# Kernel optimization log

Measured on AMD Instinct MI355X. Metric: run time of the kernel, lower is better.

## Reference

```python
import jax, jax.numpy as jnp
import numpy as np

B, S, E, H = 8, 2048, 256, 8
LN_EPS = 1e-5


def setup_inputs() -> dict:
    key = jax.random.key(0)
    ks = jax.random.split(key, 5)
    x = jax.random.normal(ks[0], (B, S, E), dtype=jnp.float32)
    Wq = jax.random.normal(ks[1], (E, E), dtype=jnp.float32) * 0.02
    Wk = jax.random.normal(ks[2], (E, E), dtype=jnp.float32) * 0.02
    Wv = jax.random.normal(ks[3], (E, E), dtype=jnp.float32) * 0.02
    bias_table = jax.random.normal(ks[4], (2 * S - 1, H), dtype=jnp.float32) * 0.02
    ln_gamma = jnp.ones((E,), dtype=jnp.float32)
    ln_beta = jnp.zeros((E,), dtype=jnp.float32)
    return {"x": x, "Wq": Wq, "Wk": Wk, "Wv": Wv,
            "bias_table": bias_table, "ln_gamma": ln_gamma, "ln_beta": ln_beta}


def reference(x, Wq, Wk, Wv, bias_table, ln_gamma, ln_beta):
    b, s, e = x.shape
    h = bias_table.shape[1]
    d = e // h
    scale = e ** (-0.5)  # note: original scales by emb_size**-0.5, not head_dim

    # torch nn.Linear(bias=False): y = x @ W.T
    q = (x @ Wq.T).reshape(b, s, h, d).transpose(0, 2, 1, 3)  # [b,h,s,d]
    k = (x @ Wk.T).reshape(b, s, h, d).transpose(0, 2, 1, 3)
    v = (x @ Wv.T).reshape(b, s, h, d).transpose(0, 2, 1, 3)

    # full attention matrix (the chunked torch loop computes exactly this)
    attn = jax.nn.softmax(jnp.einsum('bhqd,bhkd->bhqk', q, k) * scale, axis=-1)

    # relative bias: index[i,j] = i - j + (s-1); added AFTER softmax (faithful)
    idx = jnp.arange(s)[:, None] - jnp.arange(s)[None, :] + (s - 1)  # [s,s]
    rel_bias = bias_table[idx].transpose(2, 0, 1)  # [h,s,s]
    attn = attn + rel_bias[None]

    out = jnp.einsum('bhqk,bhkd->bhqd', attn, v)
    out = out.transpose(0, 2, 1, 3).reshape(b, s, e)

    # LayerNorm over last dim
    mu = jnp.mean(out, axis=-1, keepdims=True)
    var = jnp.var(out, axis=-1, keepdims=True)
    out = (out - mu) * jax.lax.rsqrt(var + LN_EPS) * ln_gamma + ln_beta
    return out
```

## Files before the change

### kernel.cpp

```cpp
#include <hip/hip_runtime.h>
#include <math.h>

typedef unsigned short u16;
typedef unsigned int u32;
typedef __attribute__((ext_vector_type(8))) short short8;
typedef __attribute__((ext_vector_type(16))) float floatx16;

constexpr int CB = 8;
constexpr int CS = 2048;
constexpr int CE = 256;
constexpr int CH = 8;
constexpr int CD = 32;
constexpr float CLN_EPS = 1e-5f;
constexpr float QSC = 0.0625f * 1.44269504088896341f;

constexpr int QP = 40;
constexpr int VP2 = 136;
constexpr int XP = 264;
constexpr int RST = 4104;

__device__ inline u32 fbits(float f) { union { float f; u32 u; } c; c.f = f; return c.u; }
__device__ inline u32 pack2(float a, float b) {
  return __builtin_amdgcn_perm(fbits(b) + 0x8000u, fbits(a) + 0x8000u, 0x07060302u);
}
__device__ inline u16 bf1(float a) { return (u16)((fbits(a) + 0x8000u) >> 16); }
__device__ inline short8 ld8(const u16* p) {
  union { uint4 q; short8 v; } c; c.q = *(const uint4*)p; return c.v;
}

#if __has_builtin(__builtin_amdgcn_permlane32_swap)
__device__ inline void swap32(u32& a, u32& b) {
  typedef __attribute__((ext_vector_type(2))) unsigned int uint2v;
  uint2v r = __builtin_amdgcn_permlane32_swap(a, b, false, false);
  a = r[0]; b = r[1];
}
#else
__device__ inline void swap32(u32& a, u32& b) {
  int hi = (threadIdx.x >> 5) & 1;
  u32 sa = (u32)__shfl_xor((int)a, 32);
  u32 sb = (u32)__shfl_xor((int)b, 32);
  u32 na = hi ? sb : a;
  u32 nb = hi ? b : sa;
  a = na; b = nb;
}
#endif

__global__ __launch_bounds__(256) void prep_kernel(
    const float* __restrict__ Wq, const float* __restrict__ Wk,
    const float* __restrict__ Wv, const float* __restrict__ table,
    u16* __restrict__ Wb, u16* __restrict__ revg) {
  int gid = blockIdx.x * 256 + threadIdx.x;
  if (gid < 49152) {
    int which = gid >> 14;
    int off = (gid & 16383) * 4;
    const float* W = (which == 0) ? Wq : (which == 1) ? Wk : Wv;
    float4 f = *(const float4*)&W[off];
    uint2 o; o.x = pack2(f.x, f.y); o.y = pack2(f.z, f.w);
    *(uint2*)&Wb[(size_t)which * CE * CE + off] = o;
  } else {
    int gid2 = gid - 49152;
    if (gid2 >= 64 * 513) return;
    int g = gid2 / 513;
    int j0 = (gid2 - g * 513) * 8;
    int h = g >> 3, p = g & 7;
    u16 vals[8];
#pragma unroll
    for (int t = 0; t < 8; ++t) {
      int src = 4094 - (j0 + t + p);
      vals[t] = (src >= 0) ? bf1(table[(size_t)src * CH + h]) : (u16)0;
    }
    *(uint4*)&revg[(size_t)g * RST + j0] = *(uint4*)vals;
  }
}

__global__ __launch_bounds__(256, 3) void qkv_mfma_kernel(
    const float* __restrict__ x, const u16* __restrict__ Wb,
    u16* __restrict__ qb, u16* __restrict__ kb, u16* __restrict__ vb) {
  __shared__ __attribute__((aligned(16))) u16 Xs[32 * XP];
  const int m0 = blockIdx.x * 32;
  const int nh = blockIdx.y;
  const int tid = threadIdx.x;
  const int lane = tid & 63, wv = tid >> 6;
  const int lm = lane & 31, lg = lane >> 5;

#pragma unroll
  for (int it = 0; it < 8; ++it) {
    int c = tid + 256 * it;
    int row = c >> 6, f4 = c & 63;
    float4 f = *(const float4*)&x[(size_t)(m0 + row) * CE + f4 * 4];
    uint2 o; o.x = pack2(f.x, f.y); o.y = pack2(f.z, f.w);
    *(uint2*)&Xs[row * XP + f4 * 4] = o;
  }
  __syncthreads();

  const int sg = m0 + lm;
  const int bI = sg >> 11, sI = sg & (CS - 1);

  for (int j = 0; j < 3; ++j) {
    int t = nh * 12 + wv * 3 + j;
    int which = t >> 3;
    int nc = (t & 7) * 32;
    int h = nc >> 5;
    const u16* Wsrc = Wb + (size_t)which * CE * CE;
    floatx16 acc;
#pragma unroll
    for (int i = 0; i < 16; ++i) acc[i] = 0.f;
#pragma unroll
    for (int half = 0; half < 2; ++half) {
      short8 wf[8], xf[8];
#pragma unroll
      for (int kt = 0; kt < 8; ++kt) {
        wf[kt] = ld8(&Wsrc[(size_t)(nc + lm) * CE + (half * 8 + kt) * 16 + lg * 8]);
        xf[kt] = ld8(&Xs[lm * XP + (half * 8 + kt) * 16 + lg * 8]);
      }
#pragma unroll
      for (int kt = 0; kt < 8; ++kt)
        acc = __builtin_amdgcn_mfma_f32_32x32x16_bf16(wf[kt], xf[kt], acc, 0, 0, 0);
    }
    if (which < 2) {
      u16* dst = which ? kb : qb;
      float scl = which ? 1.0f : QSC;
      u32 D[8];
#pragma unroll
      for (int g = 0; g < 8; ++g)
        D[g] = pack2(acc[2 * g] * scl, acc[2 * g + 1] * scl);
      swap32(D[0], D[2]); swap32(D[1], D[3]);
      swap32(D[4], D[6]); swap32(D[5], D[7]);
      size_t base = (((size_t)bI * CH + h) * CS + sI) * CD;
      uint4 U0; U0.x = D[0]; U0.y = D[1]; U0.z = D[2]; U0.w = D[3];
      uint4 U1; U1.x = D[4]; U1.y = D[5]; U1.z = D[6]; U1.w = D[7];
      *(uint4*)&dst[base + 8 * lg] = U0;
      *(uint4*)&dst[base + 16 + 8 * lg] = U1;
    } else {
#pragma unroll
      for (int r = 0; r < 16; ++r) {
        int d = (r & 3) + 8 * (r >> 2) + 4 * lg;
        vb[(((size_t)bI * CH + h) * CD + d) * CS + sI] = bf1(acc[r]);
      }
    }
  }
}

__global__ __launch_bounds__(256, 4) void attn_mfma_kernel(
    const u16* __restrict__ qm, const u16* __restrict__ km,
    const u16* __restrict__ vm, const u16* __restrict__ revg,
    float* __restrict__ out) {
  __shared__ __attribute__((aligned(16))) u16 Ks[2][128 * QP];
  __shared__ __attribute__((aligned(16))) u16 Vt[2][32 * VP2];

  const int q0 = blockIdx.x * 128;
  const int bh = blockIdx.y;
  const int b = bh >> 3, h = bh & 7;
  const int tid = threadIdx.x;
  const int lane = tid & 63, wv = tid >> 6;
  const int lm = lane & 31, lg = lane >> 5;
  const u16* qbp = qm + (size_t)bh * CS * CD;
  const u16* kbp = km + (size_t)bh * CS * CD;
  const u16* vbp = vm + (size_t)bh * CD * CS;

  const int qrow = wv * 32 + lm;
  const u16* qp = qbp + (size_t)(q0 + qrow) * CD;
  short8 qa0 = ld8(qp + lg * 8);
  short8 qa1 = ld8(qp + 16 + lg * 8);

  const int Xb = 2047 - q0 - qrow + lg * 8;
  const int pp = Xb & 7;
  const u16* bp = revg + (size_t)(h * 8 + pp) * RST + (Xb - pp);

  short8 ones;
#pragma unroll
  for (int i = 0; i < 8; ++i) ones[i] = (short)0x3F80;

  const int krow = tid >> 1, kc = (tid & 1) * 16;
  const int vrow = tid >> 3, vc = (tid & 7) * 16;
  uint4 kr0 = *(const uint4*)&kbp[(size_t)krow * CD + kc];
  uint4 kr1 = *(const uint4*)&kbp[(size_t)krow * CD + kc + 8];
  uint4 vr0 = *(const uint4*)&vbp[(size_t)vrow * CS + vc];
  uint4 vr1 = *(const uint4*)&vbp[(size_t)vrow * CS + vc + 8];

  floatx16 acc_e, acc_b, acc_l;
#pragma unroll
  for (int i = 0; i < 16; ++i) { acc_e[i] = 0.f; acc_b[i] = 0.f; acc_l[i] = 0.f; }

  for (int k0 = 0; k0 < CS; k0 += 128) {
    const int p = (k0 >> 7) & 1;
    *(uint4*)&Ks[p][krow * QP + kc] = kr0;
    *(uint4*)&Ks[p][krow * QP + kc + 8] = kr1;
    *(uint4*)&Vt[p][vrow * VP2 + vc] = vr0;
    *(uint4*)&Vt[p][vrow * VP2 + vc + 8] = vr1;
    if (k0 + 128 < CS) {
      kr0 = *(const uint4*)&kbp[(size_t)(k0 + 128 + krow) * CD + kc];
      kr1 = *(const uint4*)&kbp[(size_t)(k0 + 128 + krow) * CD + kc + 8];
      vr0 = *(const uint4*)&vbp[(size_t)vrow * CS + (k0 + 128) + vc];
      vr1 = *(const uint4*)&vbp[(size_t)vrow * CS + (k0 + 128) + vc + 8];
    }
    __syncthreads();

#pragma unroll
    for (int ct = 0; ct < 4; ++ct) {
      uint4 bua = *(const uint4*)&bp[k0 + ct * 32];
      uint4 bub = *(const uint4*)&bp[k0 + ct * 32 + 16];
      short8 a00 = ld8(&Ks[p][(ct * 32 + lm) * QP + lg * 8]);
      short8 a01 = ld8(&Ks[p][(ct * 32 + lm) * QP + 16 + lg * 8]);
      floatx16 sc;
#pragma unroll
      for (int i = 0; i < 16; ++i) sc[i] = 0.f;
      sc = __builtin_amdgcn_mfma_f32_32x32x16_bf16(a00, qa0, sc, 0, 0, 0);
      sc = __builtin_amdgcn_mfma_f32_32x32x16_bf16(a01, qa1, sc, 0, 0, 0);
      u32 P[8];
#pragma unroll
      for (int g = 0; g < 8; ++g) {
        float e0 = __builtin_amdgcn_exp2f(sc[2 * g]);
        float e1 = __builtin_amdgcn_exp2f(sc[2 * g + 1]);
        P[g] = pack2(e0, e1);
      }
      swap32(P[0], P[2]); swap32(P[1], P[3]);
      swap32(P[4], P[6]); swap32(P[5], P[7]);
      union { u32 u[4]; short8 v; } B0, B1;
      B0.u[0] = P[0]; B0.u[1] = P[1]; B0.u[2] = P[2]; B0.u[3] = P[3];
      B1.u[0] = P[4]; B1.u[1] = P[5]; B1.u[2] = P[6]; B1.u[3] = P[7];
      short8 va0 = ld8(&Vt[p][lm * VP2 + ct * 32 + lg * 8]);
      short8 va1 = ld8(&Vt[p][lm * VP2 + ct * 32 + 16 + lg * 8]);
      acc_e = __builtin_amdgcn_mfma_f32_32x32x16_bf16(va0, B0.v, acc_e, 0, 0, 0);
      acc_e = __builtin_amdgcn_mfma_f32_32x32x16_bf16(va1, B1.v, acc_e, 0, 0, 0);
      acc_l = __builtin_amdgcn_mfma_f32_32x32x16_bf16(ones, B0.v, acc_l, 0, 0, 0);
      acc_l = __builtin_amdgcn_mfma_f32_32x32x16_bf16(ones, B1.v, acc_l, 0, 0, 0);
      union { uint4 q; short8 v; } Bb0, Bb1;
      Bb0.q = bua; Bb1.q = bub;
      acc_b = __builtin_amdgcn_mfma_f32_32x32x16_bf16(va0, Bb0.v, acc_b, 0, 0, 0);
      acc_b = __builtin_amdgcn_mfma_f32_32x32x16_bf16(va1, Bb1.v, acc_b, 0, 0, 0);
    }
  }

  float rl = __builtin_amdgcn_rcpf(acc_l[0]);
  size_t ob = ((size_t)b * CS + q0 + qrow) * CE + h * CD;
#pragma unroll
  for (int g = 0; g < 4; ++g) {
    float4 r4;
    r4.x = acc_e[4 * g + 0] * rl + acc_b[4 * g + 0];
    r4.y = acc_e[4 * g + 1] * rl + acc_b[4 * g + 1];
    r4.z = acc_e[4 * g + 2] * rl + acc_b[4 * g + 2];
    r4.w = acc_e[4 * g + 3] * rl + acc_b[4 * g + 3];
    *(float4*)&out[ob + 8 * g + 4 * lg] = r4;
  }
}

__global__ __launch_bounds__(256) void ln_kernel(float* __restrict__ io,
                                                 const float* __restrict__ gamma,
                                                 const float* __restrict__ beta) {
  int tid = threadIdx.x;
  size_t row = (size_t)blockIdx.x * 4 + (tid >> 6);
  int c = (tid & 63) * 4;
  float4 v = *(const float4*)&io[row * CE + c];
  float s1 = v.x + v.y + v.z + v.w;
  float s2 = v.x * v.x + v.y * v.y + v.z * v.z + v.w * v.w;
#pragma unroll
  for (int off = 1; off < 64; off <<= 1) {
    s1 += __shfl_xor(s1, off);
    s2 += __shfl_xor(s2, off);
  }
  float mu = s1 * (1.0f / CE);
  float var = s2 * (1.0f / CE) - mu * mu;
  float rs = rsqrtf(var + CLN_EPS);
  float4 g = *(const float4*)&gamma[c];
  float4 be = *(const float4*)&beta[c];
  float4 o;
  o.x = (v.x - mu) * rs * g.x + be.x;
  o.y = (v.y - mu) * rs * g.y + be.y;
  o.z = (v.z - mu) * rs * g.z + be.z;
  o.w = (v.w - mu) * rs * g.w + be.w;
  *(float4*)&io[row * CE + c] = o;
}

extern "C" void kernel_launch(void* const* d_in, const int* in_sizes, int n_in,
                              void* d_out, int out_size, void* d_ws, size_t ws_size,
                              hipStream_t stream) {
  (void)in_sizes; (void)n_in; (void)out_size; (void)ws_size;
  const float* x          = (const float*)d_in[0];
  const float* Wq         = (const float*)d_in[1];
  const float* Wk         = (const float*)d_in[2];
  const float* Wv         = (const float*)d_in[3];
  const float* bias_table = (const float*)d_in[4];
  const float* gamma      = (const float*)d_in[5];
  const float* beta       = (const float*)d_in[6];
  float* out = (float*)d_out;

  u16* ws = (u16*)d_ws;
  u16* Wb = ws;
  u16* qb = Wb + 3 * CE * CE;
  u16* kb = qb + (size_t)CB * CH * CS * CD;
  u16* vb = kb + (size_t)CB * CH * CS * CD;
  u16* revg = vb + (size_t)CB * CH * CS * CD;

  prep_kernel<<<dim3(321), dim3(256), 0, stream>>>(Wq, Wk, Wv, bias_table, Wb, revg);
  qkv_mfma_kernel<<<dim3(512, 2), dim3(256), 0, stream>>>(x, Wb, qb, kb, vb);
  attn_mfma_kernel<<<dim3(CS / 128, CB * CH), dim3(256), 0, stream>>>(qb, kb, vb, revg, out);
  ln_kernel<<<dim3(CB * CS / 4), dim3(256), 0, stream>>>(out, gamma, beta);
}
```

Baseline: 190.8 us.

## Retile QKV GEMM with staged weights, shrink attention blocks, sum softmax denominator in registers

```diff
diff --git a/kernel.cpp b/kernel.cpp
--- a/kernel.cpp
+++ b/kernel.cpp
@@ -15,8 +15,8 @@
 constexpr float QSC = 0.0625f * 1.44269504088896341f;
 
 constexpr int QP = 40;
-constexpr int VP2 = 136;
-constexpr int XP = 264;
+constexpr int VP = 72;
+constexpr int WP = 264;
 constexpr int RST = 4104;
 
 __device__ inline u32 fbits(float f) { union { float f; u32 u; } c; c.f = f; return c.u; }
@@ -73,50 +73,72 @@
   }
 }
 
-__global__ __launch_bounds__(256, 3) void qkv_mfma_kernel(
+__global__ __launch_bounds__(256, 4) void qkv_mfma_kernel(
     const float* __restrict__ x, const u16* __restrict__ Wb,
     u16* __restrict__ qb, u16* __restrict__ kb, u16* __restrict__ vb) {
-  __shared__ __attribute__((aligned(16))) u16 Xs[32 * XP];
-  const int m0 = blockIdx.x * 32;
-  const int nh = blockIdx.y;
+  __shared__ __attribute__((aligned(16))) u16 Ws[64 * WP];
+  __shared__ __attribute__((aligned(16))) u16 Xs[2][128 * QP];
+  const int m0 = blockIdx.x * 128;
+  const int F0 = blockIdx.y * 64;
   const int tid = threadIdx.x;
   const int lane = tid & 63, wv = tid >> 6;
   const int lm = lane & 31, lg = lane >> 5;
 
-#pragma unroll
-  for (int it = 0; it < 8; ++it) {
-    int c = tid + 256 * it;
-    int row = c >> 6, f4 = c & 63;
-    float4 f = *(const float4*)&x[(size_t)(m0 + row) * CE + f4 * 4];
-    uint2 o; o.x = pack2(f.x, f.y); o.y = pack2(f.z, f.w);
-    *(uint2*)&Xs[row * XP + f4 * 4] = o;
-  }
-  __syncthreads();
-
-  const int sg = m0 + lm;
+  {
+    const u16* Wsrc = Wb + (size_t)(F0 >> 8) * CE * CE + (size_t)(F0 & 255) * CE;
+#pragma unroll
+    for (int c = 0; c < 8; ++c) {
+      int i = tid * 8 + c;
+      int row = i >> 5, col = (i & 31) * 8;
+      *(uint4*)&Ws[row * WP + col] = *(const uint4*)&Wsrc[(size_t)row * CE + col];
+    }
+  }
+
+  const int xrow = tid >> 1, xh = (tid & 1) * 16;
+  const float* xsrc = &x[(size_t)(m0 + xrow) * CE + xh];
+  float4 px0 = *(const float4*)(xsrc + 0);
+  float4 px1 = *(const float4*)(xsrc + 4);
+  float4 px2 = *(const float4*)(xsrc + 8);
+  float4 px3 = *(const float4*)(xsrc + 12);
+
+  floatx16 acc0, acc1;
+#pragma unroll
+  for (int i = 0; i < 16; ++i) { acc0[i] = 0.f; acc1[i] = 0.f; }
+
+  for (int c = 0; c < 8; ++c) {
+    const int p = c & 1;
+    uint4 u;
+    u.x = pack2(px0.x, px0.y); u.y = pack2(px0.z, px0.w);
+    u.z = pack2(px1.x, px1.y); u.w = pack2(px1.z, px1.w);
+    *(uint4*)&Xs[p][xrow * QP + xh] = u;
+    u.x = pack2(px2.x, px2.y); u.y = pack2(px2.z, px2.w);
+    u.z = pack2(px3.x, px3.y); u.w = pack2(px3.z, px3.w);
+    *(uint4*)&Xs[p][xrow * QP + xh + 8] = u;
+    if (c + 1 < 8) {
+      const float* nx = xsrc + (c + 1) * 32;
+      px0 = *(const float4*)(nx + 0);
+      px1 = *(const float4*)(nx + 4);
+      px2 = *(const float4*)(nx + 8);
+      px3 = *(const float4*)(nx + 12);
+    }
+    __syncthreads();
+#pragma unroll
+    for (int kt = 0; kt < 2; ++kt) {
+      short8 bx = ld8(&Xs[p][(wv * 32 + lm) * QP + kt * 16 + lg * 8]);
+      short8 a0 = ld8(&Ws[lm * WP + c * 32 + kt * 16 + lg * 8]);
+      short8 a1 = ld8(&Ws[(32 + lm) * WP + c * 32 + kt * 16 + lg * 8]);
+      acc0 = __builtin_amdgcn_mfma_f32_32x32x16_bf16(a0, bx, acc0, 0, 0, 0);
+      acc1 = __builtin_amdgcn_mfma_f32_32x32x16_bf16(a1, bx, acc1, 0, 0, 0);
+    }
+  }
+
+  const int sg = m0 + wv * 32 + lm;
   const int bI = sg >> 11, sI = sg & (CS - 1);
-
-  for (int j = 0; j < 3; ++j) {
-    int t = nh * 12 + wv * 3 + j;
-    int which = t >> 3;
-    int nc = (t & 7) * 32;
-    int h = nc >> 5;
-    const u16* Wsrc = Wb + (size_t)which * CE * CE;
-    floatx16 acc;
-#pragma unroll
-    for (int i = 0; i < 16; ++i) acc[i] = 0.f;
-#pragma unroll
-    for (int half = 0; half < 2; ++half) {
-      short8 wf[8], xf[8];
-#pragma unroll
-      for (int kt = 0; kt < 8; ++kt) {
-        wf[kt] = ld8(&Wsrc[(size_t)(nc + lm) * CE + (half * 8 + kt) * 16 + lg * 8]);
-        xf[kt] = ld8(&Xs[lm * XP + (half * 8 + kt) * 16 + lg * 8]);
-      }
-#pragma unroll
-      for (int kt = 0; kt < 8; ++kt)
-        acc = __builtin_amdgcn_mfma_f32_32x32x16_bf16(wf[kt], xf[kt], acc, 0, 0, 0);
-    }
+#pragma unroll
+  for (int ns = 0; ns < 2; ++ns) {
+    floatx16& acc = ns ? acc1 : acc0;
+    int F = F0 + ns * 32;
+    int which = F >> 8, hh = (F & 255) >> 5;
     if (which < 2) {
       u16* dst = which ? kb : qb;
       float scl = which ? 1.0f : QSC;
@@ -126,7 +148,7 @@
         D[g] = pack2(acc[2 * g] * scl, acc[2 * g + 1] * scl);
       swap32(D[0], D[2]); swap32(D[1], D[3]);
       swap32(D[4], D[6]); swap32(D[5], D[7]);
-      size_t base = (((size_t)bI * CH + h) * CS + sI) * CD;
+      size_t base = (((size_t)bI * CH + hh) * CS + sI) * CD;
       uint4 U0; U0.x = D[0]; U0.y = D[1]; U0.z = D[2]; U0.w = D[3];
       uint4 U1; U1.x = D[4]; U1.y = D[5]; U1.z = D[6]; U1.w = D[7];
       *(uint4*)&dst[base + 8 * lg] = U0;
@@ -135,20 +157,20 @@
 #pragma unroll
       for (int r = 0; r < 16; ++r) {
         int d = (r & 3) + 8 * (r >> 2) + 4 * lg;
-        vb[(((size_t)bI * CH + h) * CD + d) * CS + sI] = bf1(acc[r]);
+        vb[(((size_t)bI * CH + hh) * CD + d) * CS + sI] = bf1(acc[r]);
       }
     }
   }
 }
 
-__global__ __launch_bounds__(256, 4) void attn_mfma_kernel(
+__global__ __launch_bounds__(128, 4) void attn_mfma_kernel(
     const u16* __restrict__ qm, const u16* __restrict__ km,
     const u16* __restrict__ vm, const u16* __restrict__ revg,
     float* __restrict__ out) {
-  __shared__ __attribute__((aligned(16))) u16 Ks[2][128 * QP];
-  __shared__ __attribute__((aligned(16))) u16 Vt[2][32 * VP2];
-
-  const int q0 = blockIdx.x * 128;
+  __shared__ __attribute__((aligned(16))) u16 Ks[2][64 * QP];
+  __shared__ __attribute__((aligned(16))) u16 Vt[2][32 * VP];
+
+  const int q0 = blockIdx.x * 64;
   const int bh = blockIdx.y;
   const int b = bh >> 3, h = bh & 7;
   const int tid = threadIdx.x;
@@ -167,37 +189,34 @@
   const int pp = Xb & 7;
   const u16* bp = revg + (size_t)(h * 8 + pp) * RST + (Xb - pp);
 
-  short8 ones;
-#pragma unroll
-  for (int i = 0; i < 8; ++i) ones[i] = (short)0x3F80;
-
-  const int krow = tid >> 1, kc = (tid & 1) * 16;
-  const int vrow = tid >> 3, vc = (tid & 7) * 16;
-  uint4 kr0 = *(const uint4*)&kbp[(size_t)krow * CD + kc];
-  uint4 kr1 = *(const uint4*)&kbp[(size_t)krow * CD + kc + 8];
-  uint4 vr0 = *(const uint4*)&vbp[(size_t)vrow * CS + vc];
-  uint4 vr1 = *(const uint4*)&vbp[(size_t)vrow * CS + vc + 8];
-
-  floatx16 acc_e, acc_b, acc_l;
-#pragma unroll
-  for (int i = 0; i < 16; ++i) { acc_e[i] = 0.f; acc_b[i] = 0.f; acc_l[i] = 0.f; }
-
-  for (int k0 = 0; k0 < CS; k0 += 128) {
-    const int p = (k0 >> 7) & 1;
-    *(uint4*)&Ks[p][krow * QP + kc] = kr0;
-    *(uint4*)&Ks[p][krow * QP + kc + 8] = kr1;
-    *(uint4*)&Vt[p][vrow * VP2 + vc] = vr0;
-    *(uint4*)&Vt[p][vrow * VP2 + vc + 8] = vr1;
-    if (k0 + 128 < CS) {
-      kr0 = *(const uint4*)&kbp[(size_t)(k0 + 128 + krow) * CD + kc];
-      kr1 = *(const uint4*)&kbp[(size_t)(k0 + 128 + krow) * CD + kc + 8];
-      vr0 = *(const uint4*)&vbp[(size_t)vrow * CS + (k0 + 128) + vc];
-      vr1 = *(const uint4*)&vbp[(size_t)vrow * CS + (k0 + 128) + vc + 8];
+  const int krow = tid >> 1, kq = (tid & 1) * 16;
+  const int vrow = tid >> 2, vq = (tid & 3) * 16;
+  uint4 kr0 = *(const uint4*)&kbp[(size_t)krow * CD + kq];
+  uint4 kr1 = *(const uint4*)&kbp[(size_t)krow * CD + kq + 8];
+  uint4 vr0 = *(const uint4*)&vbp[(size_t)vrow * CS + vq];
+  uint4 vr1 = *(const uint4*)&vbp[(size_t)vrow * CS + vq + 8];
+
+  floatx16 acc_e, acc_b;
+#pragma unroll
+  for (int i = 0; i < 16; ++i) { acc_e[i] = 0.f; acc_b[i] = 0.f; }
+  float l = 0.f;
+
+  for (int k0 = 0; k0 < CS; k0 += 64) {
+    const int p = (k0 >> 6) & 1;
+    *(uint4*)&Ks[p][krow * QP + kq] = kr0;
+    *(uint4*)&Ks[p][krow * QP + kq + 8] = kr1;
+    *(uint4*)&Vt[p][vrow * VP + vq] = vr0;
+    *(uint4*)&Vt[p][vrow * VP + vq + 8] = vr1;
+    if (k0 + 64 < CS) {
+      kr0 = *(const uint4*)&kbp[(size_t)(k0 + 64 + krow) * CD + kq];
+      kr1 = *(const uint4*)&kbp[(size_t)(k0 + 64 + krow) * CD + kq + 8];
+      vr0 = *(const uint4*)&vbp[(size_t)vrow * CS + (k0 + 64) + vq];
+      vr1 = *(const uint4*)&vbp[(size_t)vrow * CS + (k0 + 64) + vq + 8];
     }
     __syncthreads();
 
 #pragma unroll
-    for (int ct = 0; ct < 4; ++ct) {
+    for (int ct = 0; ct < 2; ++ct) {
       uint4 bua = *(const uint4*)&bp[k0 + ct * 32];
       uint4 bub = *(const uint4*)&bp[k0 + ct * 32 + 16];
       short8 a00 = ld8(&Ks[p][(ct * 32 + lm) * QP + lg * 8]);
@@ -212,6 +231,7 @@
       for (int g = 0; g < 8; ++g) {
         float e0 = __builtin_amdgcn_exp2f(sc[2 * g]);
         float e1 = __builtin_amdgcn_exp2f(sc[2 * g + 1]);
+        l += e0 + e1;
         P[g] = pack2(e0, e1);
       }
       swap32(P[0], P[2]); swap32(P[1], P[3]);
@@ -219,12 +239,10 @@
       union { u32 u[4]; short8 v; } B0, B1;
       B0.u[0] = P[0]; B0.u[1] = P[1]; B0.u[2] = P[2]; B0.u[3] = P[3];
       B1.u[0] = P[4]; B1.u[1] = P[5]; B1.u[2] = P[6]; B1.u[3] = P[7];
-      short8 va0 = ld8(&Vt[p][lm * VP2 + ct * 32 + lg * 8]);
-      short8 va1 = ld8(&Vt[p][lm * VP2 + ct * 32 + 16 + lg * 8]);
+      short8 va0 = ld8(&Vt[p][lm * VP + ct * 32 + lg * 8]);
+      short8 va1 = ld8(&Vt[p][lm * VP + ct * 32 + 16 + lg * 8]);
       acc_e = __builtin_amdgcn_mfma_f32_32x32x16_bf16(va0, B0.v, acc_e, 0, 0, 0);
       acc_e = __builtin_amdgcn_mfma_f32_32x32x16_bf16(va1, B1.v, acc_e, 0, 0, 0);
-      acc_l = __builtin_amdgcn_mfma_f32_32x32x16_bf16(ones, B0.v, acc_l, 0, 0, 0);
-      acc_l = __builtin_amdgcn_mfma_f32_32x32x16_bf16(ones, B1.v, acc_l, 0, 0, 0);
       union { uint4 q; short8 v; } Bb0, Bb1;
       Bb0.q = bua; Bb1.q = bub;
       acc_b = __builtin_amdgcn_mfma_f32_32x32x16_bf16(va0, Bb0.v, acc_b, 0, 0, 0);
@@ -232,7 +250,8 @@
     }
   }
 
-  float rl = __builtin_amdgcn_rcpf(acc_l[0]);
+  l += __shfl_xor(l, 32);
+  float rl = __builtin_amdgcn_rcpf(l);
   size_t ob = ((size_t)b * CS + q0 + qrow) * CE + h * CD;
 #pragma unroll
   for (int g = 0; g < 4; ++g) {
@@ -293,7 +312,7 @@
   u16* revg = vb + (size_t)CB * CH * CS * CD;
 
   prep_kernel<<<dim3(321), dim3(256), 0, stream>>>(Wq, Wk, Wv, bias_table, Wb, revg);
-  qkv_mfma_kernel<<<dim3(512, 2), dim3(256), 0, stream>>>(x, Wb, qb, kb, vb);
-  attn_mfma_kernel<<<dim3(CS / 128, CB * CH), dim3(256), 0, stream>>>(qb, kb, vb, revg, out);
+  qkv_mfma_kernel<<<dim3(128, 12), dim3(256), 0, stream>>>(x, Wb, qb, kb, vb);
+  attn_mfma_kernel<<<dim3(CS / 64, CB * CH), dim3(128), 0, stream>>>(qb, kb, vb, revg, out);
   ln_kernel<<<dim3(CB * CS / 4), dim3(256), 0, stream>>>(out, gamma, beta);
 }
```

Result: faster. 183.0 us (-4.1%).
